# Kernel optimization log

Measured on AMD Instinct MI355X. Metric: run time of the kernel, lower is better.

The kernel has to match this reference:

```python
import jax, jax.numpy as jnp
import numpy as np

H = 16
D_MODEL = 1024
D_K = D_MODEL // H


def setup_inputs() -> dict:
    key = jax.random.key(0)
    ks = jax.random.split(key, 12)
    B, S = 4, 2048
    inp = {
        "query": jax.random.normal(ks[0], (B, S, D_MODEL), dtype=jnp.float32),
        "key": jax.random.normal(ks[1], (B, S, D_MODEL), dtype=jnp.float32),
        "value": jax.random.normal(ks[2], (B, S, D_MODEL), dtype=jnp.float32),
        "mask": jax.random.randint(ks[3], (B, S, S), 0, 2, dtype=jnp.int32),
    }
    # torch nn.Linear params: weight [out, in], bias [out]; y = x @ W.T + b
    scale = 1.0 / np.sqrt(D_MODEL)
    for i, name in enumerate(["q", "k", "v", "o"]):
        inp[f"W{name}"] = jax.random.uniform(ks[4 + i], (D_MODEL, D_MODEL), jnp.float32, -scale, scale)
        inp[f"b{name}"] = jax.random.uniform(ks[8 + i], (D_MODEL,), jnp.float32, -scale, scale)
    return inp


def reference(query, key, value, mask, Wq, bq, Wk, bk, Wv, bv, Wo, bo):
    B, S, _ = query.shape
    # project and split heads -> [B, H, S, D_K]
    def split_heads(x, W, b):
        return (x @ W.T + b).reshape(B, -1, H, D_K).transpose(0, 2, 1, 3)

    q = split_heads(query, Wq, bq)
    k = split_heads(key, Wk, bk)
    v = split_heads(value, Wv, bv)

    scores = jnp.einsum("bhqd,bhkd->bhqk", q, k) / jnp.sqrt(jnp.float32(D_K))
    # mask: [B, Sq, Sk] -> broadcast over heads; masked_fill(mask == 0, -1e9)
    scores = jnp.where(mask[:, None, :, :] == 0, jnp.float32(-1e9), scores)
    p_attn = jax.nn.softmax(scores, axis=-1)
    # dropout is identity in eval mode (deterministic reference)
    x = jnp.einsum("bhqk,bhkd->bhqd", p_attn, v)
    x = x.transpose(0, 2, 1, 3).reshape(B, -1, H * D_K)
    return x @ Wo.T + bo
```

## Files before the change

### kernel.cpp

```cpp
#include <hip/hip_runtime.h>
#include <stdint.h>
#include <stddef.h>


typedef __attribute__((ext_vector_type(4))) float  f32x4;
typedef __attribute__((ext_vector_type(8))) short  s16x8;
typedef __attribute__((ext_vector_type(4))) int    i32x4;

#define DEVI static __device__ __forceinline__

DEVI short f2bf(float f) {
  union { float f; uint32_t u; } c; c.f = f;
  uint32_t r = (c.u + 0x7fffu + ((c.u >> 16) & 1u)) >> 16;
  return (short)r;
}

typedef __attribute__((address_space(1))) void gvoid;
typedef __attribute__((address_space(3))) void lvoid;
#define GLL16(g, l) __builtin_amdgcn_global_load_lds((gvoid*)(g), (lvoid*)(l), 16, 0, 0)
#define MFMA(A, B, C) __builtin_amdgcn_mfma_f32_16x16x32_bf16((A), (B), (C), 0, 0, 0)

__global__ __launch_bounds__(256) void pack_mask_kernel(const int* __restrict__ mask,
                                                        uint32_t* __restrict__ bmT) {
  const int tid = blockIdx.x * 256 + threadIdx.x;
  const int q  = tid & 2047;
  const int kw = (tid >> 11) & 63;
  const int b  = tid >> 17;
  const int* src = mask + ((size_t)(b * 2048 + q)) * 2048 + (kw << 5);
  uint32_t wrd = 0;
#pragma unroll
  for (int j = 0; j < 8; ++j) {
    i32x4 v = *(const i32x4*)(src + (j << 2));
    wrd |= (v[0] ? 1u : 0u) << (j * 4 + 0);
    wrd |= (v[1] ? 1u : 0u) << (j * 4 + 1);
    wrd |= (v[2] ? 1u : 0u) << (j * 4 + 2);
    wrd |= (v[3] ? 1u : 0u) << (j * 4 + 3);
  }
  bmT[((size_t)(b * 64 + kw)) * 2048 + q] = wrd;
}

__global__ __launch_bounds__(256) void convert1_kernel(const float* __restrict__ s,
                                                       short* __restrict__ d, int n8) {
  const int i = blockIdx.x * 256 + threadIdx.x;
  if (i >= n8) return;
  f32x4 a = ((const f32x4*)s)[2 * i];
  f32x4 b = ((const f32x4*)s)[2 * i + 1];
  s16x8 o = {f2bf(a[0]), f2bf(a[1]), f2bf(a[2]), f2bf(a[3]),
             f2bf(b[0]), f2bf(b[1]), f2bf(b[2]), f2bf(b[3])};
  ((s16x8*)d)[i] = o;
}

__global__ __launch_bounds__(256) void convert4_kernel(
    const float* __restrict__ s0, short* __restrict__ d0,
    const float* __restrict__ s1, short* __restrict__ d1,
    const float* __restrict__ s2, short* __restrict__ d2,
    const float* __restrict__ s3, short* __restrict__ d3, int n8) {
  const float* s; short* d;
  switch (blockIdx.y) {
    case 0: s = s0; d = d0; break;
    case 1: s = s1; d = d1; break;
    case 2: s = s2; d = d2; break;
    default: s = s3; d = d3; break;
  }
  const int i = blockIdx.x * 256 + threadIdx.x;
  if (i >= n8) return;
  f32x4 a = ((const f32x4*)s)[2 * i];
  f32x4 b = ((const f32x4*)s)[2 * i + 1];
  s16x8 o = {f2bf(a[0]), f2bf(a[1]), f2bf(a[2]), f2bf(a[3]),
             f2bf(b[0]), f2bf(b[1]), f2bf(b[2]), f2bf(b[3])};
  ((s16x8*)d)[i] = o;
}

template <bool OUT_F32>
__global__ __launch_bounds__(256, 2) void gemm_bias_kernel(
    const short* __restrict__ A, const short* __restrict__ W,
    const float* __restrict__ bias, void* __restrict__ Yp,
    const int M, const int N, const int K) {
  __shared__ short As[128 * 32];
  __shared__ short Bs[128 * 32];
  const int t = threadIdx.x;
  const int lane = t & 63, w = t >> 6;
  const int wm = w >> 1, wn = w & 1;
  const int l15 = lane & 15, lg = lane >> 4;
  const int m0 = blockIdx.y * 128, n0 = blockIdx.x * 128;

  f32x4 acc[4][4];
#pragma unroll
  for (int m = 0; m < 4; ++m)
#pragma unroll
    for (int n = 0; n < 4; ++n) acc[m][n] = f32x4{0.f, 0.f, 0.f, 0.f};

  const int srow = t >> 2, scol = (t & 3) << 3;

  for (int kt = 0; kt < K; kt += 32) {
    __syncthreads();
    GLL16(A + (size_t)(m0 + srow) * K + kt + scol, &As[t * 8]);
    GLL16(A + (size_t)(m0 + 64 + srow) * K + kt + scol, &As[2048 + t * 8]);
    GLL16(W + (size_t)(n0 + srow) * K + kt + scol, &Bs[t * 8]);
    GLL16(W + (size_t)(n0 + 64 + srow) * K + kt + scol, &Bs[2048 + t * 8]);
    __syncthreads();

    s16x8 af[4], bf[4];
#pragma unroll
    for (int m = 0; m < 4; ++m)
      af[m] = *(const s16x8*)(&As[(wm * 64 + m * 16 + l15) * 32 + lg * 8]);
#pragma unroll
    for (int n = 0; n < 4; ++n)
      bf[n] = *(const s16x8*)(&Bs[(wn * 64 + n * 16 + l15) * 32 + lg * 8]);
#pragma unroll
    for (int m = 0; m < 4; ++m)
#pragma unroll
      for (int n = 0; n < 4; ++n) acc[m][n] = MFMA(af[m], bf[n], acc[m][n]);
  }

  float bn[4];
#pragma unroll
  for (int n = 0; n < 4; ++n) bn[n] = bias[n0 + wn * 64 + n * 16 + l15];
#pragma unroll
  for (int m = 0; m < 4; ++m) {
    const int row = m0 + wm * 64 + m * 16 + lg * 4;
#pragma unroll
    for (int n = 0; n < 4; ++n) {
      const int col = n0 + wn * 64 + n * 16 + l15;
#pragma unroll
      for (int r = 0; r < 4; ++r) {
        const float v = acc[m][n][r] + bn[n];
        if constexpr (OUT_F32)
          ((float*)Yp)[(size_t)(row + r) * N + col] = v;
        else
          ((short*)Yp)[(size_t)(row + r) * N + col] = f2bf(v);
      }
    }
  }
}

__global__ __launch_bounds__(256) void attn_kernel(
    const short* __restrict__ qb, const short* __restrict__ kb,
    const short* __restrict__ vb, const uint32_t* __restrict__ bmT,
    short* __restrict__ xb) {
  __shared__ short Ks[32 * 64];
  __shared__ uint32_t Vt[64 * 20];
  __shared__ uint32_t Mw[64];
  __shared__ short Ps[4][16 * 40];

  const int t = threadIdx.x;
  const int lane = t & 63, w = t >> 6;
  const int l15 = lane & 15, lg = lane >> 4;
  const int b = blockIdx.z, h = blockIdx.y, q0 = blockIdx.x * 64;

  const short* qrow = qb + ((size_t)(b * 2048 + q0 + w * 16 + l15)) * 1024 + h * 64;
  const s16x8 qf0 = *(const s16x8*)(qrow + lg * 8);
  const s16x8 qf1 = *(const s16x8*)(qrow + 32 + lg * 8);

  float lsum[4] = {0.f, 0.f, 0.f, 0.f};
  f32x4 accO[4];
#pragma unroll
  for (int n = 0; n < 4; ++n) accO[n] = f32x4{0.f, 0.f, 0.f, 0.f};

  const short* kbase = kb + ((size_t)(b * 2048)) * 1024 + h * 64;
  const short* vbase = vb + ((size_t)(b * 2048)) * 1024 + h * 64;
  const uint32_t* mbase = bmT + (size_t)(b * 64) * 2048 + q0;

  const float CEXP = 0.125f * 1.44269504f;

  const int vk2 = t >> 4, vm = t & 15;

  for (int kt = 0; kt < 2048; kt += 32) {
    __syncthreads();
    {
      const int krow = t >> 3;
      const int gsw = (((t & 7) ^ (krow & 7)) << 3);
      GLL16(kbase + (size_t)(kt + krow) * 1024 + gsw, &Ks[t * 8]);
    }
    {
      const short* v0p = vbase + (size_t)(kt + 2 * vk2) * 1024;
      const short* v1p = v0p + 1024;
#pragma unroll
      for (int i = 0; i < 4; ++i) {
        const int d = vm + 16 * i;
        const uint32_t lo = (uint16_t)v0p[d], hi = (uint16_t)v1p[d];
        Vt[d * 20 + vk2] = lo | (hi << 16);
      }
    }
    if (t < 64) Mw[t] = mbase[(size_t)(kt >> 5) * 2048 + t];
    __syncthreads();

    f32x4 s0, s1;
    {
      const f32x4 z = {0.f, 0.f, 0.f, 0.f};
      const int sx = l15 & 7;
      const s16x8 k00 = *(const s16x8*)(&Ks[(l15) * 64 + (((0 + lg) ^ sx) << 3)]);
      const s16x8 k01 = *(const s16x8*)(&Ks[(l15) * 64 + (((4 + lg) ^ sx) << 3)]);
      const s16x8 k10 = *(const s16x8*)(&Ks[(16 + l15) * 64 + (((0 + lg) ^ sx) << 3)]);
      const s16x8 k11 = *(const s16x8*)(&Ks[(16 + l15) * 64 + (((4 + lg) ^ sx) << 3)]);
      s0 = MFMA(qf0, k00, z);
      s0 = MFMA(qf1, k01, s0);
      s1 = MFMA(qf0, k10, z);
      s1 = MFMA(qf1, k11, s1);
    }

#pragma unroll
    for (int r = 0; r < 4; ++r) {
      const uint32_t wd = Mw[w * 16 + lg * 4 + r];
      const float p0 = ((wd >> l15) & 1u) ? exp2f(s0[r] * CEXP) : 0.f;
      const float p1 = ((wd >> (16 + l15)) & 1u) ? exp2f(s1[r] * CEXP) : 0.f;
      lsum[r] += p0 + p1;
      short* pr = &Ps[w][(lg * 4 + r) * 40];
      pr[l15] = f2bf(p0);
      pr[16 + l15] = f2bf(p1);
    }

    const s16x8 pf = *(const s16x8*)(&Ps[w][l15 * 40 + lg * 8]);
#pragma unroll
    for (int n = 0; n < 4; ++n) {
      const s16x8 vf = *(const s16x8*)((const short*)&Vt[(n * 16 + l15) * 20] + lg * 8);
      accO[n] = MFMA(pf, vf, accO[n]);
    }
  }

#pragma unroll
  for (int r = 0; r < 4; ++r) {
    float sp = lsum[r];
    sp += __shfl_xor(sp, 1, 16);
    sp += __shfl_xor(sp, 2, 16);
    sp += __shfl_xor(sp, 4, 16);
    sp += __shfl_xor(sp, 8, 16);
    const float inv = 1.0f / sp;
    short* dst = xb + ((size_t)(b * 2048 + q0 + w * 16 + lg * 4 + r)) * 1024 + h * 64;
#pragma unroll
    for (int n = 0; n < 4; ++n) dst[n * 16 + l15] = f2bf(accO[n][r] * inv);
  }
}

extern "C" void kernel_launch(void* const* d_in, const int* in_sizes, int n_in,
                              void* d_out, int out_size, void* d_ws, size_t ws_size,
                              hipStream_t stream) {
  const float* q_in = (const float*)d_in[0];
  const float* k_in = (const float*)d_in[1];
  const float* v_in = (const float*)d_in[2];
  const int* mask   = (const int*)d_in[3];
  const float* Wq = (const float*)d_in[4];
  const float* bq = (const float*)d_in[5];
  const float* Wk = (const float*)d_in[6];
  const float* bk = (const float*)d_in[7];
  const float* Wv = (const float*)d_in[8];
  const float* bv = (const float*)d_in[9];
  const float* Wo = (const float*)d_in[10];
  const float* bo = (const float*)d_in[11];

  char* ws = (char*)d_ws;
  const size_t SZ = (size_t)8192 * 1024 * 2;
  const size_t WSZ = (size_t)1024 * 1024 * 2;
  short* qb = (short*)(ws);
  short* kb = (short*)(ws + SZ);
  short* vb = (short*)(ws + 2 * SZ);
  short* tc = (short*)(ws + 3 * SZ);
  uint32_t* bm = (uint32_t*)(ws + 4 * SZ);
  short* Wqc = (short*)(ws + 4 * SZ + 2 * WSZ);
  short* Wkc = Wqc + (size_t)1024 * 1024;
  short* Wvc = Wkc + (size_t)1024 * 1024;
  short* Woc = Wvc + (size_t)1024 * 1024;

  const int N8IN = 8192 * 1024 / 8, N8W = 1024 * 1024 / 8;

  pack_mask_kernel<<<2048, 256, 0, stream>>>(mask, bm);
  convert4_kernel<<<dim3(N8W / 256, 4), 256, 0, stream>>>(Wq, Wqc, Wk, Wkc, Wv, Wvc, Wo, Woc, N8W);

  convert1_kernel<<<N8IN / 256, 256, 0, stream>>>(q_in, tc, N8IN);
  gemm_bias_kernel<false><<<dim3(8, 64), 256, 0, stream>>>(tc, Wqc, bq, qb, 8192, 1024, 1024);
  convert1_kernel<<<N8IN / 256, 256, 0, stream>>>(k_in, tc, N8IN);
  gemm_bias_kernel<false><<<dim3(8, 64), 256, 0, stream>>>(tc, Wkc, bk, kb, 8192, 1024, 1024);
  convert1_kernel<<<N8IN / 256, 256, 0, stream>>>(v_in, tc, N8IN);
  gemm_bias_kernel<false><<<dim3(8, 64), 256, 0, stream>>>(tc, Wvc, bv, vb, 8192, 1024, 1024);

  attn_kernel<<<dim3(32, 16, 4), 256, 0, stream>>>(qb, kb, vb, bm, tc);
  gemm_bias_kernel<true><<<dim3(8, 64), 256, 0, stream>>>(tc, Woc, bo, d_out, 8192, 1024, 1024);
}
```

Before: 506.8 us.

## Process 64 keys per barrier pair and pack P with hardware bf16 convert

Doubles the key tile per iteration to 64 rows, staging two 32-key halves of K, V and mask per sync, which halves the __syncthreads count. P values are now packed as interleaved pairs with v_cvt_pk_bf16_f32 instead of software rounding, and V pairing changes to keys k and k+16 to match that P layout. Also swaps exp2f with folded scale for __expf. LDS usage grows and the P/V key ordering changes, which must stay consistent for correctness.

Measured after the change: 472.7 us. 6.7% less time.

```diff
diff --git a/kernel.cpp b/kernel.cpp
--- a/kernel.cpp
+++ b/kernel.cpp
@@ -138,10 +138,10 @@
     const short* __restrict__ qb, const short* __restrict__ kb,
     const short* __restrict__ vb, const uint32_t* __restrict__ bmT,
     short* __restrict__ xb) {
-  __shared__ short Ks[32 * 64];
-  __shared__ uint32_t Vt[64 * 20];
-  __shared__ uint32_t Mw[64];
-  __shared__ short Ps[4][16 * 40];
+  __shared__ short Ks[64 * 64];
+  __shared__ uint32_t Vt[2][64 * 20];
+  __shared__ uint32_t Mw[2][64];
+  __shared__ uint32_t Ps[4][16 * 20];
 
   const int t = threadIdx.x;
   const int lane = t & 63, w = t >> 6;
@@ -161,60 +161,61 @@
   const short* vbase = vb + ((size_t)(b * 2048)) * 1024 + h * 64;
   const uint32_t* mbase = bmT + (size_t)(b * 64) * 2048 + q0;
 
-  const float CEXP = 0.125f * 1.44269504f;
-
+  const float SC = 0.125f;
   const int vk2 = t >> 4, vm = t & 15;
-
-  for (int kt = 0; kt < 2048; kt += 32) {
-    __syncthreads();
-    {
-      const int krow = t >> 3;
-      const int gsw = (((t & 7) ^ (krow & 7)) << 3);
-      GLL16(kbase + (size_t)(kt + krow) * 1024 + gsw, &Ks[t * 8]);
-    }
-    {
-      const short* v0p = vbase + (size_t)(kt + 2 * vk2) * 1024;
-      const short* v1p = v0p + 1024;
+  const int krow = t >> 3;
+  const int gsw = (((t & 7) ^ (krow & 7)) << 3);
+  const int sx = l15 & 7;
+
+  for (int kt = 0; kt < 2048; kt += 64) {
+    __syncthreads();
+    GLL16(kbase + (size_t)(kt + krow) * 1024 + gsw, &Ks[t * 8]);
+    GLL16(kbase + (size_t)(kt + 32 + krow) * 1024 + gsw, &Ks[2048 + t * 8]);
+#pragma unroll
+    for (int hh = 0; hh < 2; ++hh) {
+      const short* v0p = vbase + (size_t)(kt + 32 * hh + vk2) * 1024;
+      const short* v1p = v0p + 16 * 1024;
 #pragma unroll
       for (int i = 0; i < 4; ++i) {
         const int d = vm + 16 * i;
         const uint32_t lo = (uint16_t)v0p[d], hi = (uint16_t)v1p[d];
-        Vt[d * 20 + vk2] = lo | (hi << 16);
+        Vt[hh][d * 20 + vk2] = lo | (hi << 16);
       }
     }
-    if (t < 64) Mw[t] = mbase[(size_t)(kt >> 5) * 2048 + t];
-    __syncthreads();
-
-    f32x4 s0, s1;
-    {
-      const f32x4 z = {0.f, 0.f, 0.f, 0.f};
-      const int sx = l15 & 7;
-      const s16x8 k00 = *(const s16x8*)(&Ks[(l15) * 64 + (((0 + lg) ^ sx) << 3)]);
-      const s16x8 k01 = *(const s16x8*)(&Ks[(l15) * 64 + (((4 + lg) ^ sx) << 3)]);
-      const s16x8 k10 = *(const s16x8*)(&Ks[(16 + l15) * 64 + (((0 + lg) ^ sx) << 3)]);
-      const s16x8 k11 = *(const s16x8*)(&Ks[(16 + l15) * 64 + (((4 + lg) ^ sx) << 3)]);
-      s0 = MFMA(qf0, k00, z);
-      s0 = MFMA(qf1, k01, s0);
-      s1 = MFMA(qf0, k10, z);
-      s1 = MFMA(qf1, k11, s1);
-    }
-
-#pragma unroll
-    for (int r = 0; r < 4; ++r) {
-      const uint32_t wd = Mw[w * 16 + lg * 4 + r];
-      const float p0 = ((wd >> l15) & 1u) ? exp2f(s0[r] * CEXP) : 0.f;
-      const float p1 = ((wd >> (16 + l15)) & 1u) ? exp2f(s1[r] * CEXP) : 0.f;
-      lsum[r] += p0 + p1;
-      short* pr = &Ps[w][(lg * 4 + r) * 40];
-      pr[l15] = f2bf(p0);
-      pr[16 + l15] = f2bf(p1);
-    }
-
-    const s16x8 pf = *(const s16x8*)(&Ps[w][l15 * 40 + lg * 8]);
-#pragma unroll
-    for (int n = 0; n < 4; ++n) {
-      const s16x8 vf = *(const s16x8*)((const short*)&Vt[(n * 16 + l15) * 20] + lg * 8);
-      accO[n] = MFMA(pf, vf, accO[n]);
+    if (t < 128) Mw[t >> 6][t & 63] = mbase[(size_t)((kt >> 5) + (t >> 6)) * 2048 + (t & 63)];
+    __syncthreads();
+
+#pragma unroll
+    for (int hh = 0; hh < 2; ++hh) {
+      const short* ksh = &Ks[hh * 2048];
+      f32x4 sa, sb;
+      {
+        const f32x4 z = {0.f, 0.f, 0.f, 0.f};
+        const s16x8 k00 = *(const s16x8*)(&ksh[(l15) * 64 + (((0 + lg) ^ sx) << 3)]);
+        const s16x8 k01 = *(const s16x8*)(&ksh[(l15) * 64 + (((4 + lg) ^ sx) << 3)]);
+        const s16x8 k10 = *(const s16x8*)(&ksh[(16 + l15) * 64 + (((0 + lg) ^ sx) << 3)]);
+        const s16x8 k11 = *(const s16x8*)(&ksh[(16 + l15) * 64 + (((4 + lg) ^ sx) << 3)]);
+        sa = MFMA(qf0, k00, z);
+        sa = MFMA(qf1, k01, sa);
+        sb = MFMA(qf0, k10, z);
+        sb = MFMA(qf1, k11, sb);
+      }
+#pragma unroll
+      for (int r = 0; r < 4; ++r) {
+        const uint32_t wd = Mw[hh][w * 16 + lg * 4 + r];
+        const float pa = ((wd >> l15) & 1u) ? __expf(sa[r] * SC) : 0.f;
+        const float pb = ((wd >> (16 + l15)) & 1u) ? __expf(sb[r] * SC) : 0.f;
+        lsum[r] += pa + pb;
+        uint32_t pw;
+        asm("v_cvt_pk_bf16_f32 %0, %1, %2" : "=v"(pw) : "v"(pa), "v"(pb));
+        Ps[w][(lg * 4 + r) * 20 + l15] = pw;
+      }
+      const s16x8 pf = *(const s16x8*)(&Ps[w][l15 * 20 + lg * 4]);
+#pragma unroll
+      for (int n = 0; n < 4; ++n) {
+        const s16x8 vf = *(const s16x8*)(&Vt[hh][(n * 16 + l15) * 20 + lg * 4]);
+        accO[n] = MFMA(pf, vf, accO[n]);
+      }
     }
   }
 
```
